# Performance work log

Measured on AMD Instinct MI355X. Metric: run time of the kernel, lower is better.

Reference implementation:

```python
import jax, jax.numpy as jnp
import numpy as np

FP16_MIN = -65504.0  # torch.finfo(torch.float16).min


def addcoords(x):
    # x: (b, c, h, w) NCHW. AddCoords(rank=1, with_r=True): appends a
    # y-coordinate channel (normalized over h, broadcast over w) and |y-0.5|.
    b, c, h, w = x.shape
    yy = (jnp.arange(h, dtype=x.dtype) / (h - 1)) * 2.0 - 1.0  # (h,)
    yy = jnp.broadcast_to(yy[None, None, :, None], (b, 1, h, w))
    rr = jnp.abs(yy - 0.5)
    return jnp.concatenate([x, yy, rr], axis=1)


def conv1x1(x, W, b):
    # W: (c_out, c_in), b: (c_out,)
    return jnp.einsum('bihw,oi->bohw', x, W) + b[None, :, None, None]


def setup_inputs() -> dict:
    key = jax.random.key(0)
    ks = jax.random.split(key, 16)
    c = 64
    B2, h, w = 4, 256, 256
    s_in = 0.02
    inp = {
        'x': jax.random.normal(ks[0], (B2, c, h, w), jnp.float32),
        'res_enc': jax.random.normal(ks[1], (B2, c, h, w), jnp.float32),
        'tr_feat': jax.random.normal(ks[2], (B2, c, h, w), jnp.float32),
        # CoordConv 1x1 weights take c+2 input channels (coord + r channels)
        'Wl1': jax.random.normal(ks[3], (c, c + 2), jnp.float32) * s_in,
        'bl1': jax.random.normal(ks[4], (c,), jnp.float32) * s_in,
        'Wr1': jax.random.normal(ks[5], (c, c + 2), jnp.float32) * s_in,
        'br1': jax.random.normal(ks[6], (c,), jnp.float32) * s_in,
        'Wl2': jax.random.normal(ks[7], (c, c), jnp.float32) * s_in,
        'bl2': jax.random.normal(ks[8], (c,), jnp.float32) * s_in,
        'Wr2': jax.random.normal(ks[9], (c, c), jnp.float32) * s_in,
        'br2': jax.random.normal(ks[10], (c,), jnp.float32) * s_in,
        'beta1': jax.random.normal(ks[11], (1, c, 1, 1), jnp.float32) * s_in,
        'gamma1': jax.random.normal(ks[12], (1, c, 1, 1), jnp.float32) * s_in,
        'beta3': jax.random.normal(ks[13], (1, c, 1, 1), jnp.float32) * s_in,
        'gamma3': jax.random.normal(ks[14], (1, c, 1, 1), jnp.float32) * s_in,
    }
    return inp


def reference(x, res_enc, tr_feat, Wl1, bl1, Wr1, br1, Wl2, bl2, Wr2, br2,
              beta1, gamma1, beta3, gamma3):
    x_l, x_r = jnp.split(x, 2, axis=0)
    re_l, re_r = jnp.split(res_enc, 2, axis=0)
    tr_l, tr_r = jnp.split(tr_feat, 2, axis=0)
    b, c, h, w = x_l.shape
    scale = jnp.asarray(c, x.dtype) ** -0.5

    Q = conv1x1(addcoords(x_l), Wl1, bl1) + beta1 * tr_l   # (b, c, h, w)
    S = conv1x1(addcoords(x_r), Wr1, br1) + beta1 * tr_r   # (b, c, h, w)

    # per-row (epipolar) attention along width: score[b,h,i,j]
    score = jnp.einsum('bchi,bchj->bhij', Q, S) * scale
    idx = jnp.arange(w)
    upper = idx[None, :] > idx[:, None]  # strict upper triangle (j > i)
    score = jnp.where(upper[None, None], FP16_MIN, score)
    # In torch, score_T is a view of score; after in-place masking, score_T
    # masked at strict-lower positions == transpose of masked score.
    M_r2l = jax.nn.softmax(score, axis=-1)                       # (b,h,w,w)
    M_l2r = jax.nn.softmax(jnp.swapaxes(score, -1, -2), axis=-1)  # (b,h,w,w)

    buf_R = conv1x1(x_r, Wr2, br2) + gamma1 * re_r  # (b, c, h, w)
    buf_l = jnp.einsum('bhij,bchj->bchi', M_r2l, buf_R)
    buf_L = conv1x1(x_l, Wl2, bl2) + gamma1 * re_l
    buf_r = jnp.einsum('bhij,bchj->bchi', M_l2r, buf_L)

    out_L = x_l + beta3 * buf_l
    out_R = x_r + gamma3 * buf_r
    return jnp.concatenate([out_L, out_R], axis=0)
```

## Files before the change

### kernel.cpp

```cpp
#include <hip/hip_runtime.h>
#include <stdint.h>

#define HW 65536
#define C_ 64

typedef __attribute__((ext_vector_type(8))) short short8;
typedef __attribute__((ext_vector_type(4))) float f32x4;

#define MFMA(a, b, c) __builtin_amdgcn_mfma_f32_16x16x32_bf16((a), (b), (c), 0, 0, 0)

union U16x8 { uint4 q; short8 v; uint32_t u[4]; };

__device__ inline uint32_t pack_bf16(float lo, float hi) {
  uint32_t ul = __float_as_uint(lo), uh = __float_as_uint(hi);
  ul = (ul + 0x7fffu + ((ul >> 16) & 1u)) >> 16;
  uh = (uh + 0x7fffu + ((uh >> 16) & 1u)) >> 16;
  return ul | (uh << 16);
}
__device__ inline uint16_t bf16r(float f) {
  uint32_t u = __float_as_uint(f);
  return (uint16_t)((u + 0x7fffu + ((u >> 16) & 1u)) >> 16);
}
__device__ inline short8 ld8(const uint16_t* p) {
  U16x8 t; t.q = *(const uint4*)p; return t.v;
}
__device__ inline int pc_idx(int pixel, int c) {
  return (pixel * 64 + c) ^ ((pixel & 7) << 3);
}
__device__ inline int cj_idx(int c, int j) {
  return (c * 256 + j) ^ ((c & 7) << 3);
}

__global__ __launch_bounds__(512, 1) void SCAM_73151882985874_kernel(
    const float* __restrict__ x, const float* __restrict__ res_enc,
    const float* __restrict__ tr_feat,
    const float* __restrict__ Wl1, const float* __restrict__ bl1,
    const float* __restrict__ Wr1, const float* __restrict__ br1,
    const float* __restrict__ Wl2, const float* __restrict__ bl2,
    const float* __restrict__ Wr2, const float* __restrict__ br2,
    const float* __restrict__ beta1, const float* __restrict__ gamma1,
    const float* __restrict__ beta3, const float* __restrict__ gamma3,
    float* __restrict__ out)
{
  __shared__ uint16_t sX[16384];
  __shared__ uint16_t sQ[16384];
  __shared__ uint16_t sS[16384];
  __shared__ uint16_t sV[16384];
  __shared__ uint16_t sP[10240];

  const int tid = threadIdx.x;
  const int wid = tid >> 6, lane = tid & 63, g = lane >> 4, li = lane & 15;
  const int bb = blockIdx.x >> 8, hh = blockIdx.x & 255;
  const float yy = (float)hh * (2.0f / 255.0f) - 1.0f;
  const float rr = fabsf(yy - 0.5f);

  const size_t rowoff = (size_t)hh * 256;
  const float* xl  = x + ((size_t)bb * C_) * HW + rowoff;
  const float* xr  = x + ((size_t)(2 + bb) * C_) * HW + rowoff;
  const float* trl = tr_feat + ((size_t)bb * C_) * HW + rowoff;
  const float* trr = tr_feat + ((size_t)(2 + bb) * C_) * HW + rowoff;
  const float* rel = res_enc + ((size_t)bb * C_) * HW + rowoff;
  const float* rer = res_enc + ((size_t)(2 + bb) * C_) * HW + rowoff;
  float* outL = out + ((size_t)bb * C_) * HW + rowoff;
  float* outR = out + ((size_t)(2 + bb) * C_) * HW + rowoff;

  uint16_t* Pw = &sP[wid * 1280];

  auto stage = [&](const float* src) {
    int p = tid & 255, h = tid >> 8;
    #pragma unroll
    for (int cb = 0; cb < 4; ++cb) {
      int c0 = h * 32 + cb * 8;
      const float* s = src + (size_t)c0 * HW + p;
      U16x8 t;
      t.u[0] = pack_bf16(s[0],              s[(size_t)HW]);
      t.u[1] = pack_bf16(s[2 * (size_t)HW], s[3 * (size_t)HW]);
      t.u[2] = pack_bf16(s[4 * (size_t)HW], s[5 * (size_t)HW]);
      t.u[3] = pack_bf16(s[6 * (size_t)HW], s[7 * (size_t)HW]);
      *(uint4*)&sX[pc_idx(p, c0)] = t.q;
    }
  };

  auto conv = [&](const float* Wm, int ldw, const float* bias, const float* mod,
                  const float* E, int coord, float qscale,
                  uint16_t* dstQ , int toV) {
    short8 af[4][2];
    #pragma unroll
    for (int ct = 0; ct < 4; ++ct)
      #pragma unroll
      for (int kk = 0; kk < 2; ++kk) {
        const float* wr = Wm + (size_t)(ct * 16 + li) * ldw + kk * 32 + g * 8;
        U16x8 t;
        t.u[0] = pack_bf16(wr[0], wr[1]);
        t.u[1] = pack_bf16(wr[2], wr[3]);
        t.u[2] = pack_bf16(wr[4], wr[5]);
        t.u[3] = pack_bf16(wr[6], wr[7]);
        af[ct][kk] = t.v;
      }
    #pragma unroll
    for (int ptl = 0; ptl < 2; ++ptl) {
      int pix = (wid * 2 + ptl) * 16 + li;
      short8 bx0 = ld8(&sX[pc_idx(pix, g * 8)]);
      short8 bx1 = ld8(&sX[pc_idx(pix, 32 + g * 8)]);
      #pragma unroll
      for (int ct = 0; ct < 4; ++ct) {
        f32x4 acc = {0.f, 0.f, 0.f, 0.f};
        acc = MFMA(af[ct][0], bx0, acc);
        acc = MFMA(af[ct][1], bx1, acc);
        uint16_t pk[4];
        #pragma unroll
        for (int r = 0; r < 4; ++r) {
          int c = ct * 16 + 4 * g + r;
          float b = bias[c];
          if (coord) b += Wm[(size_t)c * ldw + 64] * yy + Wm[(size_t)c * ldw + 65] * rr;
          float v = (acc[r] + b + mod[c] * E[(size_t)c * HW + pix]) * qscale;
          pk[r] = bf16r(v);
          if (toV) sV[cj_idx(c, pix)] = pk[r];
        }
        if (!toV) {
          uint2 w2;
          w2.x = (uint32_t)pk[0] | ((uint32_t)pk[1] << 16);
          w2.y = (uint32_t)pk[2] | ((uint32_t)pk[3] << 16);
          *(uint2*)&dstQ[pc_idx(pix, ct * 16 + 4 * g)] = w2;
        }
      }
    }
  };

  stage(xl);
  __syncthreads();
  conv(Wl1, 66, bl1, beta1, trl, 1, 0.125f, sQ, 0);
  conv(Wl2, 64, bl2, gamma1, rel, 0, 1.0f, nullptr, 1);
  __syncthreads();
  stage(xr);
  __syncthreads();
  conv(Wr1, 66, br1, beta1, trr, 1, 1.0f, sS, 0);
  __syncthreads();

  {
    const int j0 = wid * 32;
    short8 bS[2][2];
    #pragma unroll
    for (int jt = 0; jt < 2; ++jt)
      #pragma unroll
      for (int kk = 0; kk < 2; ++kk)
        bS[jt][kk] = ld8(&sS[pc_idx(j0 + jt * 16 + li, kk * 32 + g * 8)]);

    f32x4 acc[4][2];
    #pragma unroll
    for (int ct = 0; ct < 4; ++ct) { acc[ct][0] = (f32x4){0,0,0,0}; acc[ct][1] = (f32x4){0,0,0,0}; }
    float zp0 = 0.f, zp1 = 0.f;

    for (int ip = wid; ip < 8; ++ip) {
      #pragma unroll
      for (int itl = 0; itl < 2; ++itl) {
        short8 aQ0 = ld8(&sQ[pc_idx(ip * 32 + itl * 16 + li, g * 8)]);
        short8 aQ1 = ld8(&sQ[pc_idx(ip * 32 + itl * 16 + li, 32 + g * 8)]);
        #pragma unroll
        for (int jt = 0; jt < 2; ++jt) {
          f32x4 s = {0.f, 0.f, 0.f, 0.f};
          s = MFMA(aQ0, bS[jt][0], s);
          s = MFMA(aQ1, bS[jt][1], s);
          int jj = j0 + jt * 16 + li;
          float ps = 0.f; uint16_t pk[4];
          #pragma unroll
          for (int r = 0; r < 4; ++r) {
            int ii = ip * 32 + itl * 16 + 4 * g + r;
            float p = (ii >= jj) ? __expf(s[r]) : 0.f;
            ps += p; pk[r] = bf16r(p);
          }
          if (jt == 0) zp0 += ps; else zp1 += ps;
          uint2 w2;
          w2.x = (uint32_t)pk[0] | ((uint32_t)pk[1] << 16);
          w2.y = (uint32_t)pk[2] | ((uint32_t)pk[3] << 16);
          *(uint2*)&Pw[(jt * 16 + li) * 40 + itl * 16 + 4 * g] = w2;
        }
      }
      #pragma unroll
      for (int jt = 0; jt < 2; ++jt) {
        short8 bP = ld8(&Pw[(jt * 16 + li) * 40 + 8 * g]);
        #pragma unroll
        for (int ct = 0; ct < 4; ++ct) {
          short8 aV = ld8(&sV[cj_idx(ct * 16 + li, ip * 32 + 8 * g)]);
          acc[ct][jt] = MFMA(aV, bP, acc[ct][jt]);
        }
      }
    }
    zp0 += __shfl_xor(zp0, 16); zp0 += __shfl_xor(zp0, 32);
    zp1 += __shfl_xor(zp1, 16); zp1 += __shfl_xor(zp1, 32);
    #pragma unroll
    for (int jt = 0; jt < 2; ++jt) {
      float invz = 1.0f / (jt == 0 ? zp0 : zp1);
      int j = j0 + jt * 16 + li;
      #pragma unroll
      for (int ct = 0; ct < 4; ++ct)
        #pragma unroll
        for (int r = 0; r < 4; ++r) {
          int c = ct * 16 + 4 * g + r;
          outR[(size_t)c * HW + j] =
              fmaf(gamma3[c], acc[ct][jt][r] * invz, xr[(size_t)c * HW + j]);
        }
    }
  }
  __syncthreads();
  conv(Wr2, 64, br2, gamma1, rer, 0, 1.0f, nullptr, 1);
  __syncthreads();

  {
    const int i0 = wid * 32;
    short8 bQ[2][2];
    #pragma unroll
    for (int itl = 0; itl < 2; ++itl)
      #pragma unroll
      for (int kk = 0; kk < 2; ++kk)
        bQ[itl][kk] = ld8(&sQ[pc_idx(i0 + itl * 16 + li, kk * 32 + g * 8)]);

    f32x4 acc[4][2];
    #pragma unroll
    for (int ct = 0; ct < 4; ++ct) { acc[ct][0] = (f32x4){0,0,0,0}; acc[ct][1] = (f32x4){0,0,0,0}; }
    float zp0 = 0.f, zp1 = 0.f;

    for (int jp = 0; jp <= wid; ++jp) {
      #pragma unroll
      for (int jt = 0; jt < 2; ++jt) {
        short8 aS0 = ld8(&sS[pc_idx(jp * 32 + jt * 16 + li, g * 8)]);
        short8 aS1 = ld8(&sS[pc_idx(jp * 32 + jt * 16 + li, 32 + g * 8)]);
        #pragma unroll
        for (int itl = 0; itl < 2; ++itl) {
          f32x4 s = {0.f, 0.f, 0.f, 0.f};
          s = MFMA(aS0, bQ[itl][0], s);
          s = MFMA(aS1, bQ[itl][1], s);
          int ii = i0 + itl * 16 + li;
          float ps = 0.f; uint16_t pk[4];
          #pragma unroll
          for (int r = 0; r < 4; ++r) {
            int jj = jp * 32 + jt * 16 + 4 * g + r;
            float p = (jj <= ii) ? __expf(s[r]) : 0.f;
            ps += p; pk[r] = bf16r(p);
          }
          if (itl == 0) zp0 += ps; else zp1 += ps;
          uint2 w2;
          w2.x = (uint32_t)pk[0] | ((uint32_t)pk[1] << 16);
          w2.y = (uint32_t)pk[2] | ((uint32_t)pk[3] << 16);
          *(uint2*)&Pw[(itl * 16 + li) * 40 + jt * 16 + 4 * g] = w2;
        }
      }
      #pragma unroll
      for (int itl = 0; itl < 2; ++itl) {
        short8 bP = ld8(&Pw[(itl * 16 + li) * 40 + 8 * g]);
        #pragma unroll
        for (int ct = 0; ct < 4; ++ct) {
          short8 aV = ld8(&sV[cj_idx(ct * 16 + li, jp * 32 + 8 * g)]);
          acc[ct][itl] = MFMA(aV, bP, acc[ct][itl]);
        }
      }
    }
    zp0 += __shfl_xor(zp0, 16); zp0 += __shfl_xor(zp0, 32);
    zp1 += __shfl_xor(zp1, 16); zp1 += __shfl_xor(zp1, 32);
    #pragma unroll
    for (int itl = 0; itl < 2; ++itl) {
      float invz = 1.0f / (itl == 0 ? zp0 : zp1);
      int i = i0 + itl * 16 + li;
      #pragma unroll
      for (int ct = 0; ct < 4; ++ct)
        #pragma unroll
        for (int r = 0; r < 4; ++r) {
          int c = ct * 16 + 4 * g + r;
          outL[(size_t)c * HW + i] =
              fmaf(beta3[c], acc[ct][itl][r] * invz, xl[(size_t)c * HW + i]);
        }
    }
  }
}

extern "C" void kernel_launch(void* const* d_in, const int* in_sizes, int n_in,
                              void* d_out, int out_size, void* d_ws, size_t ws_size,
                              hipStream_t stream) {
  const float* x       = (const float*)d_in[0];
  const float* res_enc = (const float*)d_in[1];
  const float* tr_feat = (const float*)d_in[2];
  const float* Wl1     = (const float*)d_in[3];
  const float* bl1     = (const float*)d_in[4];
  const float* Wr1     = (const float*)d_in[5];
  const float* br1     = (const float*)d_in[6];
  const float* Wl2     = (const float*)d_in[7];
  const float* bl2     = (const float*)d_in[8];
  const float* Wr2     = (const float*)d_in[9];
  const float* br2     = (const float*)d_in[10];
  const float* beta1   = (const float*)d_in[11];
  const float* gamma1  = (const float*)d_in[12];
  const float* beta3   = (const float*)d_in[13];
  const float* gamma3  = (const float*)d_in[14];
  float* outp = (float*)d_out;

  dim3 grid(512);
  dim3 block(512);
  SCAM_73151882985874_kernel<<<grid, block, 0, stream>>>(
      x, res_enc, tr_feat, Wl1, bl1, Wr1, br1, Wl2, bl2, Wr2, br2,
      beta1, gamma1, beta3, gamma3, outp);
}
```

Measured before the change: 86.53 us.

## Use 1024-thread blocks with one 16-pixel tile per wave and merged phases

Doubles the block to 1024 threads so each wave handles a single 16-pixel tile. Both x_l and x_r are staged into shared memory at once, and all four 1x1 convolutions run in one phase, with Q and S written in place over the staged inputs. This drops several block-wide barriers and the second staging pass, and adds more waves per CU to hide latency. In exchange it uses more registers per CU, the causal triangle work is split less evenly across waves, and the launch bound now asks for 4 blocks per CU, which the shared-memory footprint may not permit.

After: 106.3 us. 22.9% more time.

```diff
diff --git a/kernel.cpp b/kernel.cpp
--- a/kernel.cpp
+++ b/kernel.cpp
@@ -31,7 +31,7 @@
   return (c * 256 + j) ^ ((c & 7) << 3);
 }
 
-__global__ __launch_bounds__(512, 1) void SCAM_73151882985874_kernel(
+__global__ __launch_bounds__(1024, 4) void SCAM_73151882985874_kernel(
     const float* __restrict__ x, const float* __restrict__ res_enc,
     const float* __restrict__ tr_feat,
     const float* __restrict__ Wl1, const float* __restrict__ bl1,
@@ -42,10 +42,10 @@
     const float* __restrict__ beta3, const float* __restrict__ gamma3,
     float* __restrict__ out)
 {
-  __shared__ uint16_t sX[16384];
-  __shared__ uint16_t sQ[16384];
-  __shared__ uint16_t sS[16384];
-  __shared__ uint16_t sV[16384];
+  __shared__ uint16_t R1[16384];
+  __shared__ uint16_t R2[16384];
+  __shared__ uint16_t R3[16384];
+  __shared__ uint16_t R4[16384];
   __shared__ uint16_t sP[10240];
 
   const int tid = threadIdx.x;
@@ -64,212 +64,180 @@
   float* outL = out + ((size_t)bb * C_) * HW + rowoff;
   float* outR = out + ((size_t)(2 + bb) * C_) * HW + rowoff;
 
-  uint16_t* Pw = &sP[wid * 1280];
-
-  auto stage = [&](const float* src) {
-    int p = tid & 255, h = tid >> 8;
+  {
+    const int side = tid >> 9;
+    const int t    = tid & 511;
+    const int p    = t & 255, h2 = t >> 8;
+    const float* src = side ? xr : xl;
+    uint16_t* dst = side ? R2 : R1;
     #pragma unroll
     for (int cb = 0; cb < 4; ++cb) {
-      int c0 = h * 32 + cb * 8;
+      int c0 = h2 * 32 + cb * 8;
       const float* s = src + (size_t)c0 * HW + p;
-      U16x8 t;
-      t.u[0] = pack_bf16(s[0],              s[(size_t)HW]);
-      t.u[1] = pack_bf16(s[2 * (size_t)HW], s[3 * (size_t)HW]);
-      t.u[2] = pack_bf16(s[4 * (size_t)HW], s[5 * (size_t)HW]);
-      t.u[3] = pack_bf16(s[6 * (size_t)HW], s[7 * (size_t)HW]);
-      *(uint4*)&sX[pc_idx(p, c0)] = t.q;
+      U16x8 t8;
+      t8.u[0] = pack_bf16(s[0],              s[(size_t)HW]);
+      t8.u[1] = pack_bf16(s[2 * (size_t)HW], s[3 * (size_t)HW]);
+      t8.u[2] = pack_bf16(s[4 * (size_t)HW], s[5 * (size_t)HW]);
+      t8.u[3] = pack_bf16(s[6 * (size_t)HW], s[7 * (size_t)HW]);
+      *(uint4*)&dst[pc_idx(p, c0)] = t8.q;
+    }
+  }
+  __syncthreads();
+
+  const int pix = wid * 16 + li;
+
+  short8 bxL0 = ld8(&R1[pc_idx(pix, g * 8)]);
+  short8 bxL1 = ld8(&R1[pc_idx(pix, 32 + g * 8)]);
+  short8 bxR0 = ld8(&R2[pc_idx(pix, g * 8)]);
+  short8 bxR1 = ld8(&R2[pc_idx(pix, 32 + g * 8)]);
+
+  auto conv_one = [&](const float* __restrict__ Wm, int ldw,
+                      const float* __restrict__ bias, const float* __restrict__ mod,
+                      const float* __restrict__ E, int coord, float qscale,
+                      short8 bx0, short8 bx1,
+                      uint16_t* dstPC, uint16_t* dstV) {
+    #pragma unroll
+    for (int ct = 0; ct < 4; ++ct) {
+      float ev[4], be[4];
+      #pragma unroll
+      for (int r = 0; r < 4; ++r) {
+        int c = ct * 16 + 4 * g + r;
+        ev[r] = E[(size_t)c * HW + pix];
+        float b = bias[c] + mod[c] * 0.0f;
+        if (coord) b += Wm[(size_t)c * ldw + 64] * yy + Wm[(size_t)c * ldw + 65] * rr;
+        be[r] = b;
+      }
+      float md[4];
+      #pragma unroll
+      for (int r = 0; r < 4; ++r) md[r] = mod[ct * 16 + 4 * g + r];
+      short8 af0, af1;
+      {
+        const float* wr = Wm + (size_t)(ct * 16 + li) * ldw + g * 8;
+        U16x8 t8;
+        t8.u[0] = pack_bf16(wr[0], wr[1]); t8.u[1] = pack_bf16(wr[2], wr[3]);
+        t8.u[2] = pack_bf16(wr[4], wr[5]); t8.u[3] = pack_bf16(wr[6], wr[7]);
+        af0 = t8.v;
+        const float* wr2 = wr + 32;
+        t8.u[0] = pack_bf16(wr2[0], wr2[1]); t8.u[1] = pack_bf16(wr2[2], wr2[3]);
+        t8.u[2] = pack_bf16(wr2[4], wr2[5]); t8.u[3] = pack_bf16(wr2[6], wr2[7]);
+        af1 = t8.v;
+      }
+      f32x4 acc = {0.f, 0.f, 0.f, 0.f};
+      acc = MFMA(af0, bx0, acc);
+      acc = MFMA(af1, bx1, acc);
+      uint16_t pk[4];
+      #pragma unroll
+      for (int r = 0; r < 4; ++r)
+        pk[r] = bf16r((acc[r] + be[r] + md[r] * ev[r]) * qscale);
+      if (dstV) {
+        #pragma unroll
+        for (int r = 0; r < 4; ++r) dstV[cj_idx(ct * 16 + 4 * g + r, pix)] = pk[r];
+      } else {
+        uint2 w2;
+        w2.x = (uint32_t)pk[0] | ((uint32_t)pk[1] << 16);
+        w2.y = (uint32_t)pk[2] | ((uint32_t)pk[3] << 16);
+        *(uint2*)&dstPC[pc_idx(pix, ct * 16 + 4 * g)] = w2;
+      }
     }
   };
 
-  auto conv = [&](const float* Wm, int ldw, const float* bias, const float* mod,
-                  const float* E, int coord, float qscale,
-                  uint16_t* dstQ , int toV) {
-    short8 af[4][2];
-    #pragma unroll
-    for (int ct = 0; ct < 4; ++ct)
-      #pragma unroll
-      for (int kk = 0; kk < 2; ++kk) {
-        const float* wr = Wm + (size_t)(ct * 16 + li) * ldw + kk * 32 + g * 8;
-        U16x8 t;
-        t.u[0] = pack_bf16(wr[0], wr[1]);
-        t.u[1] = pack_bf16(wr[2], wr[3]);
-        t.u[2] = pack_bf16(wr[4], wr[5]);
-        t.u[3] = pack_bf16(wr[6], wr[7]);
-        af[ct][kk] = t.v;
-      }
-    #pragma unroll
-    for (int ptl = 0; ptl < 2; ++ptl) {
-      int pix = (wid * 2 + ptl) * 16 + li;
-      short8 bx0 = ld8(&sX[pc_idx(pix, g * 8)]);
-      short8 bx1 = ld8(&sX[pc_idx(pix, 32 + g * 8)]);
-      #pragma unroll
-      for (int ct = 0; ct < 4; ++ct) {
-        f32x4 acc = {0.f, 0.f, 0.f, 0.f};
-        acc = MFMA(af[ct][0], bx0, acc);
-        acc = MFMA(af[ct][1], bx1, acc);
+  conv_one(Wl1, 66, bl1, beta1, trl, 1, 0.125f, bxL0, bxL1, R1, nullptr);
+  conv_one(Wr1, 66, br1, beta1, trr, 1, 1.0f,   bxR0, bxR1, R2, nullptr);
+  conv_one(Wl2, 64, bl2, gamma1, rel, 0, 1.0f,  bxL0, bxL1, nullptr, R3);
+  conv_one(Wr2, 64, br2, gamma1, rer, 0, 1.0f,  bxR0, bxR1, nullptr, R4);
+  __syncthreads();
+
+  uint16_t* Pw = &sP[wid * 640];
+  const int h = wid >> 1;
+
+  {
+    short8 bS0 = ld8(&R2[pc_idx(pix, g * 8)]);
+    short8 bS1 = ld8(&R2[pc_idx(pix, 32 + g * 8)]);
+    f32x4 acc[4] = {{0,0,0,0},{0,0,0,0},{0,0,0,0},{0,0,0,0}};
+    float z = 0.f;
+    for (int ip = h; ip < 8; ++ip) {
+      #pragma unroll
+      for (int itl = 0; itl < 2; ++itl) {
+        int arow = ip * 32 + itl * 16 + li;
+        short8 aQ0 = ld8(&R1[pc_idx(arow, g * 8)]);
+        short8 aQ1 = ld8(&R1[pc_idx(arow, 32 + g * 8)]);
+        f32x4 s = {0.f, 0.f, 0.f, 0.f};
+        s = MFMA(aQ0, bS0, s);
+        s = MFMA(aQ1, bS1, s);
         uint16_t pk[4];
         #pragma unroll
         for (int r = 0; r < 4; ++r) {
-          int c = ct * 16 + 4 * g + r;
-          float b = bias[c];
-          if (coord) b += Wm[(size_t)c * ldw + 64] * yy + Wm[(size_t)c * ldw + 65] * rr;
-          float v = (acc[r] + b + mod[c] * E[(size_t)c * HW + pix]) * qscale;
-          pk[r] = bf16r(v);
-          if (toV) sV[cj_idx(c, pix)] = pk[r];
+          int aidx = ip * 32 + itl * 16 + 4 * g + r;
+          float p = (aidx >= pix) ? __expf(s[r]) : 0.f;
+          z += p; pk[r] = bf16r(p);
         }
-        if (!toV) {
-          uint2 w2;
-          w2.x = (uint32_t)pk[0] | ((uint32_t)pk[1] << 16);
-          w2.y = (uint32_t)pk[2] | ((uint32_t)pk[3] << 16);
-          *(uint2*)&dstQ[pc_idx(pix, ct * 16 + 4 * g)] = w2;
-        }
-      }
-    }
-  };
-
-  stage(xl);
-  __syncthreads();
-  conv(Wl1, 66, bl1, beta1, trl, 1, 0.125f, sQ, 0);
-  conv(Wl2, 64, bl2, gamma1, rel, 0, 1.0f, nullptr, 1);
-  __syncthreads();
-  stage(xr);
-  __syncthreads();
-  conv(Wr1, 66, br1, beta1, trr, 1, 1.0f, sS, 0);
-  __syncthreads();
+        uint2 w2;
+        w2.x = (uint32_t)pk[0] | ((uint32_t)pk[1] << 16);
+        w2.y = (uint32_t)pk[2] | ((uint32_t)pk[3] << 16);
+        *(uint2*)&Pw[li * 40 + itl * 16 + 4 * g] = w2;
+      }
+      short8 bP = ld8(&Pw[li * 40 + 8 * g]);
+      #pragma unroll
+      for (int ct = 0; ct < 4; ++ct) {
+        short8 aV = ld8(&R3[cj_idx(ct * 16 + li, ip * 32 + 8 * g)]);
+        acc[ct] = MFMA(aV, bP, acc[ct]);
+      }
+    }
+    z += __shfl_xor(z, 16); z += __shfl_xor(z, 32);
+    float invz = 1.0f / z;
+    #pragma unroll
+    for (int ct = 0; ct < 4; ++ct)
+      #pragma unroll
+      for (int r = 0; r < 4; ++r) {
+        int c = ct * 16 + 4 * g + r;
+        outR[(size_t)c * HW + pix] =
+            fmaf(gamma3[c], acc[ct][r] * invz, xr[(size_t)c * HW + pix]);
+      }
+  }
 
   {
-    const int j0 = wid * 32;
-    short8 bS[2][2];
-    #pragma unroll
-    for (int jt = 0; jt < 2; ++jt)
-      #pragma unroll
-      for (int kk = 0; kk < 2; ++kk)
-        bS[jt][kk] = ld8(&sS[pc_idx(j0 + jt * 16 + li, kk * 32 + g * 8)]);
-
-    f32x4 acc[4][2];
-    #pragma unroll
-    for (int ct = 0; ct < 4; ++ct) { acc[ct][0] = (f32x4){0,0,0,0}; acc[ct][1] = (f32x4){0,0,0,0}; }
-    float zp0 = 0.f, zp1 = 0.f;
-
-    for (int ip = wid; ip < 8; ++ip) {
+    short8 bQ0 = ld8(&R1[pc_idx(pix, g * 8)]);
+    short8 bQ1 = ld8(&R1[pc_idx(pix, 32 + g * 8)]);
+    f32x4 acc[4] = {{0,0,0,0},{0,0,0,0},{0,0,0,0},{0,0,0,0}};
+    float z = 0.f;
+    for (int jp = 0; jp <= h; ++jp) {
       #pragma unroll
       for (int itl = 0; itl < 2; ++itl) {
-        short8 aQ0 = ld8(&sQ[pc_idx(ip * 32 + itl * 16 + li, g * 8)]);
-        short8 aQ1 = ld8(&sQ[pc_idx(ip * 32 + itl * 16 + li, 32 + g * 8)]);
-        #pragma unroll
-        for (int jt = 0; jt < 2; ++jt) {
-          f32x4 s = {0.f, 0.f, 0.f, 0.f};
-          s = MFMA(aQ0, bS[jt][0], s);
-          s = MFMA(aQ1, bS[jt][1], s);
-          int jj = j0 + jt * 16 + li;
-          float ps = 0.f; uint16_t pk[4];
-          #pragma unroll
-          for (int r = 0; r < 4; ++r) {
-            int ii = ip * 32 + itl * 16 + 4 * g + r;
-            float p = (ii >= jj) ? __expf(s[r]) : 0.f;
-            ps += p; pk[r] = bf16r(p);
-          }
-          if (jt == 0) zp0 += ps; else zp1 += ps;
-          uint2 w2;
-          w2.x = (uint32_t)pk[0] | ((uint32_t)pk[1] << 16);
-          w2.y = (uint32_t)pk[2] | ((uint32_t)pk[3] << 16);
-          *(uint2*)&Pw[(jt * 16 + li) * 40 + itl * 16 + 4 * g] = w2;
-        }
-      }
-      #pragma unroll
-      for (int jt = 0; jt < 2; ++jt) {
-        short8 bP = ld8(&Pw[(jt * 16 + li) * 40 + 8 * g]);
-        #pragma unroll
-        for (int ct = 0; ct < 4; ++ct) {
-          short8 aV = ld8(&sV[cj_idx(ct * 16 + li, ip * 32 + 8 * g)]);
-          acc[ct][jt] = MFMA(aV, bP, acc[ct][jt]);
-        }
-      }
-    }
-    zp0 += __shfl_xor(zp0, 16); zp0 += __shfl_xor(zp0, 32);
-    zp1 += __shfl_xor(zp1, 16); zp1 += __shfl_xor(zp1, 32);
-    #pragma unroll
-    for (int jt = 0; jt < 2; ++jt) {
-      float invz = 1.0f / (jt == 0 ? zp0 : zp1);
-      int j = j0 + jt * 16 + li;
-      #pragma unroll
-      for (int ct = 0; ct < 4; ++ct)
+        int arow = jp * 32 + itl * 16 + li;
+        short8 aS0 = ld8(&R2[pc_idx(arow, g * 8)]);
+        short8 aS1 = ld8(&R2[pc_idx(arow, 32 + g * 8)]);
+        f32x4 s = {0.f, 0.f, 0.f, 0.f};
+        s = MFMA(aS0, bQ0, s);
+        s = MFMA(aS1, bQ1, s);
+        uint16_t pk[4];
         #pragma unroll
         for (int r = 0; r < 4; ++r) {
-          int c = ct * 16 + 4 * g + r;
-          outR[(size_t)c * HW + j] =
-              fmaf(gamma3[c], acc[ct][jt][r] * invz, xr[(size_t)c * HW + j]);
+          int jidx = jp * 32 + itl * 16 + 4 * g + r;
+          float p = (jidx <= pix) ? __expf(s[r]) : 0.f;
+          z += p; pk[r] = bf16r(p);
         }
-    }
-  }
-  __syncthreads();
-  conv(Wr2, 64, br2, gamma1, rer, 0, 1.0f, nullptr, 1);
-  __syncthreads();
-
-  {
-    const int i0 = wid * 32;
-    short8 bQ[2][2];
-    #pragma unroll
-    for (int itl = 0; itl < 2; ++itl)
-      #pragma unroll
-      for (int kk = 0; kk < 2; ++kk)
-        bQ[itl][kk] = ld8(&sQ[pc_idx(i0 + itl * 16 + li, kk * 32 + g * 8)]);
-
-    f32x4 acc[4][2];
-    #pragma unroll
-    for (int ct = 0; ct < 4; ++ct) { acc[ct][0] = (f32x4){0,0,0,0}; acc[ct][1] = (f32x4){0,0,0,0}; }
-    float zp0 = 0.f, zp1 = 0.f;
-
-    for (int jp = 0; jp <= wid; ++jp) {
-      #pragma unroll
-      for (int jt = 0; jt < 2; ++jt) {
-        short8 aS0 = ld8(&sS[pc_idx(jp * 32 + jt * 16 + li, g * 8)]);
-        short8 aS1 = ld8(&sS[pc_idx(jp * 32 + jt * 16 + li, 32 + g * 8)]);
-        #pragma unroll
-        for (int itl = 0; itl < 2; ++itl) {
-          f32x4 s = {0.f, 0.f, 0.f, 0.f};
-          s = MFMA(aS0, bQ[itl][0], s);
-          s = MFMA(aS1, bQ[itl][1], s);
-          int ii = i0 + itl * 16 + li;
-          float ps = 0.f; uint16_t pk[4];
-          #pragma unroll
-          for (int r = 0; r < 4; ++r) {
-            int jj = jp * 32 + jt * 16 + 4 * g + r;
-            float p = (jj <= ii) ? __expf(s[r]) : 0.f;
-            ps += p; pk[r] = bf16r(p);
-          }
-          if (itl == 0) zp0 += ps; else zp1 += ps;
-          uint2 w2;
-          w2.x = (uint32_t)pk[0] | ((uint32_t)pk[1] << 16);
-          w2.y = (uint32_t)pk[2] | ((uint32_t)pk[3] << 16);
-          *(uint2*)&Pw[(itl * 16 + li) * 40 + jt * 16 + 4 * g] = w2;
-        }
-      }
-      #pragma unroll
-      for (int itl = 0; itl < 2; ++itl) {
-        short8 bP = ld8(&Pw[(itl * 16 + li) * 40 + 8 * g]);
-        #pragma unroll
-        for (int ct = 0; ct < 4; ++ct) {
-          short8 aV = ld8(&sV[cj_idx(ct * 16 + li, jp * 32 + 8 * g)]);
-          acc[ct][itl] = MFMA(aV, bP, acc[ct][itl]);
-        }
-      }
-    }
-    zp0 += __shfl_xor(zp0, 16); zp0 += __shfl_xor(zp0, 32);
-    zp1 += __shfl_xor(zp1, 16); zp1 += __shfl_xor(zp1, 32);
-    #pragma unroll
-    for (int itl = 0; itl < 2; ++itl) {
-      float invz = 1.0f / (itl == 0 ? zp0 : zp1);
-      int i = i0 + itl * 16 + li;
-      #pragma unroll
-      for (int ct = 0; ct < 4; ++ct)
-        #pragma unroll
-        for (int r = 0; r < 4; ++r) {
-          int c = ct * 16 + 4 * g + r;
-          outL[(size_t)c * HW + i] =
-              fmaf(beta3[c], acc[ct][itl][r] * invz, xl[(size_t)c * HW + i]);
-        }
-    }
+        uint2 w2;
+        w2.x = (uint32_t)pk[0] | ((uint32_t)pk[1] << 16);
+        w2.y = (uint32_t)pk[2] | ((uint32_t)pk[3] << 16);
+        *(uint2*)&Pw[li * 40 + itl * 16 + 4 * g] = w2;
+      }
+      short8 bP = ld8(&Pw[li * 40 + 8 * g]);
+      #pragma unroll
+      for (int ct = 0; ct < 4; ++ct) {
+        short8 aV = ld8(&R4[cj_idx(ct * 16 + li, jp * 32 + 8 * g)]);
+        acc[ct] = MFMA(aV, bP, acc[ct]);
+      }
+    }
+    z += __shfl_xor(z, 16); z += __shfl_xor(z, 32);
+    float invz = 1.0f / z;
+    #pragma unroll
+    for (int ct = 0; ct < 4; ++ct)
+      #pragma unroll
+      for (int r = 0; r < 4; ++r) {
+        int c = ct * 16 + 4 * g + r;
+        outL[(size_t)c * HW + pix] =
+            fmaf(beta3[c], acc[ct][r] * invz, xl[(size_t)c * HW + pix]);
+      }
   }
 }
 
@@ -294,7 +262,7 @@
   float* outp = (float*)d_out;
 
   dim3 grid(512);
-  dim3 block(512);
+  dim3 block(1024);
   SCAM_73151882985874_kernel<<<grid, block, 0, stream>>>(
       x, res_enc, tr_feat, Wl1, bl1, Wr1, br1, Wl2, bl2, Wr2, br2,
       beta1, gamma1, beta3, gamma3, outp);
```

## Prepack bf16 weights, stage both sides at once, compute all convs upfront

Applied to the files above, without the earlier changes.

Adds a small pre-kernel that converts the four conv weight matrices to bf16 in workspace, so the main kernel loads them directly instead of converting per block. Both x_l and x_r are staged into shared memory concurrently, and all four 1x1 convs are computed before attention, which removes several block-wide barriers and the mid-kernel conv. It also hoists the bias and modulation loads, batches the A/V fragment loads in the attention loops, and raises launch bounds to 2 blocks per CU. The cost is an extra launch and higher register pressure under the tighter launch bound. LDS use (about 148 KB per block) may still allow only one block per CU.

Result: slower. 92.60 us (+7.0%).

```diff
diff --git a/kernel.cpp b/kernel.cpp
--- a/kernel.cpp
+++ b/kernel.cpp
@@ -31,7 +31,18 @@
   return (c * 256 + j) ^ ((c & 7) << 3);
 }
 
-__global__ __launch_bounds__(512, 1) void SCAM_73151882985874_kernel(
+__global__ void SCAM_pack_w(const float* __restrict__ Wl1, const float* __restrict__ Wr1,
+                            const float* __restrict__ Wl2, const float* __restrict__ Wr2,
+                            uint16_t* __restrict__ ws) {
+  int idx = blockIdx.x * 256 + threadIdx.x;
+  int r = idx >> 6, k = idx & 63;
+  ws[idx]         = bf16r(Wl1[r * 66 + k]);
+  ws[4096 + idx]  = bf16r(Wr1[r * 66 + k]);
+  ws[8192 + idx]  = bf16r(Wl2[r * 64 + k]);
+  ws[12288 + idx] = bf16r(Wr2[r * 64 + k]);
+}
+
+__global__ __launch_bounds__(512, 2) void SCAM_73151882985874_kernel(
     const float* __restrict__ x, const float* __restrict__ res_enc,
     const float* __restrict__ tr_feat,
     const float* __restrict__ Wl1, const float* __restrict__ bl1,
@@ -40,12 +51,13 @@
     const float* __restrict__ Wr2, const float* __restrict__ br2,
     const float* __restrict__ beta1, const float* __restrict__ gamma1,
     const float* __restrict__ beta3, const float* __restrict__ gamma3,
+    const uint16_t* __restrict__ wsW,
     float* __restrict__ out)
 {
-  __shared__ uint16_t sX[16384];
-  __shared__ uint16_t sQ[16384];
-  __shared__ uint16_t sS[16384];
-  __shared__ uint16_t sV[16384];
+  __shared__ uint16_t R1[16384];
+  __shared__ uint16_t R2[16384];
+  __shared__ uint16_t R3[16384];
+  __shared__ uint16_t R4[16384];
   __shared__ uint16_t sP[10240];
 
   const int tid = threadIdx.x;
@@ -64,109 +76,129 @@
   float* outL = out + ((size_t)bb * C_) * HW + rowoff;
   float* outR = out + ((size_t)(2 + bb) * C_) * HW + rowoff;
 
-  uint16_t* Pw = &sP[wid * 1280];
-
-  auto stage = [&](const float* src) {
-    int p = tid & 255, h = tid >> 8;
-    #pragma unroll
-    for (int cb = 0; cb < 4; ++cb) {
-      int c0 = h * 32 + cb * 8;
+  {
+    const int side = tid >> 8;
+    const int p    = tid & 255;
+    const float* src = side ? xr : xl;
+    uint16_t* dst = side ? R2 : R1;
+    #pragma unroll
+    for (int cb = 0; cb < 8; ++cb) {
+      int c0 = cb * 8;
       const float* s = src + (size_t)c0 * HW + p;
-      U16x8 t;
-      t.u[0] = pack_bf16(s[0],              s[(size_t)HW]);
-      t.u[1] = pack_bf16(s[2 * (size_t)HW], s[3 * (size_t)HW]);
-      t.u[2] = pack_bf16(s[4 * (size_t)HW], s[5 * (size_t)HW]);
-      t.u[3] = pack_bf16(s[6 * (size_t)HW], s[7 * (size_t)HW]);
-      *(uint4*)&sX[pc_idx(p, c0)] = t.q;
-    }
-  };
-
-  auto conv = [&](const float* Wm, int ldw, const float* bias, const float* mod,
-                  const float* E, int coord, float qscale,
-                  uint16_t* dstQ , int toV) {
+      U16x8 t8;
+      t8.u[0] = pack_bf16(s[0],              s[(size_t)HW]);
+      t8.u[1] = pack_bf16(s[2 * (size_t)HW], s[3 * (size_t)HW]);
+      t8.u[2] = pack_bf16(s[4 * (size_t)HW], s[5 * (size_t)HW]);
+      t8.u[3] = pack_bf16(s[6 * (size_t)HW], s[7 * (size_t)HW]);
+      *(uint4*)&dst[pc_idx(p, c0)] = t8.q;
+    }
+  }
+  __syncthreads();
+
+  short8 bxL[2][2], bxR[2][2];
+  #pragma unroll
+  for (int ptl = 0; ptl < 2; ++ptl) {
+    int pix = wid * 32 + ptl * 16 + li;
+    bxL[ptl][0] = ld8(&R1[pc_idx(pix, g * 8)]);
+    bxL[ptl][1] = ld8(&R1[pc_idx(pix, 32 + g * 8)]);
+    bxR[ptl][0] = ld8(&R2[pc_idx(pix, g * 8)]);
+    bxR[ptl][1] = ld8(&R2[pc_idx(pix, 32 + g * 8)]);
+  }
+
+  auto conv_one = [&](const uint16_t* __restrict__ wcore,
+                      const float* __restrict__ Wc,
+                      const float* __restrict__ bias, const float* __restrict__ mod,
+                      const float* __restrict__ E, float qscale,
+                      const short8 bx[2][2], uint16_t* dstPC, uint16_t* dstV) {
     short8 af[4][2];
     #pragma unroll
+    for (int ct = 0; ct < 4; ++ct) {
+      const uint16_t* wr = wcore + (size_t)(ct * 16 + li) * 64 + g * 8;
+      af[ct][0] = ld8(wr);
+      af[ct][1] = ld8(wr + 32);
+    }
+    float be[4][4], md[4][4];
+    #pragma unroll
     for (int ct = 0; ct < 4; ++ct)
       #pragma unroll
-      for (int kk = 0; kk < 2; ++kk) {
-        const float* wr = Wm + (size_t)(ct * 16 + li) * ldw + kk * 32 + g * 8;
-        U16x8 t;
-        t.u[0] = pack_bf16(wr[0], wr[1]);
-        t.u[1] = pack_bf16(wr[2], wr[3]);
-        t.u[2] = pack_bf16(wr[4], wr[5]);
-        t.u[3] = pack_bf16(wr[6], wr[7]);
-        af[ct][kk] = t.v;
+      for (int r = 0; r < 4; ++r) {
+        int c = ct * 16 + 4 * g + r;
+        float b = bias[c];
+        if (Wc) b += Wc[(size_t)c * 66 + 64] * yy + Wc[(size_t)c * 66 + 65] * rr;
+        be[ct][r] = b;
+        md[ct][r] = mod[c];
       }
     #pragma unroll
     for (int ptl = 0; ptl < 2; ++ptl) {
-      int pix = (wid * 2 + ptl) * 16 + li;
-      short8 bx0 = ld8(&sX[pc_idx(pix, g * 8)]);
-      short8 bx1 = ld8(&sX[pc_idx(pix, 32 + g * 8)]);
+      int pix = wid * 32 + ptl * 16 + li;
       #pragma unroll
       for (int ct = 0; ct < 4; ++ct) {
+        float ev[4];
+        #pragma unroll
+        for (int r = 0; r < 4; ++r)
+          ev[r] = E[(size_t)(ct * 16 + 4 * g + r) * HW + pix];
         f32x4 acc = {0.f, 0.f, 0.f, 0.f};
-        acc = MFMA(af[ct][0], bx0, acc);
-        acc = MFMA(af[ct][1], bx1, acc);
+        acc = MFMA(af[ct][0], bx[ptl][0], acc);
+        acc = MFMA(af[ct][1], bx[ptl][1], acc);
         uint16_t pk[4];
         #pragma unroll
-        for (int r = 0; r < 4; ++r) {
-          int c = ct * 16 + 4 * g + r;
-          float b = bias[c];
-          if (coord) b += Wm[(size_t)c * ldw + 64] * yy + Wm[(size_t)c * ldw + 65] * rr;
-          float v = (acc[r] + b + mod[c] * E[(size_t)c * HW + pix]) * qscale;
-          pk[r] = bf16r(v);
-          if (toV) sV[cj_idx(c, pix)] = pk[r];
-        }
-        if (!toV) {
+        for (int r = 0; r < 4; ++r)
+          pk[r] = bf16r((acc[r] + be[ct][r] + md[ct][r] * ev[r]) * qscale);
+        if (dstV) {
+          #pragma unroll
+          for (int r = 0; r < 4; ++r) dstV[cj_idx(ct * 16 + 4 * g + r, pix)] = pk[r];
+        } else {
           uint2 w2;
           w2.x = (uint32_t)pk[0] | ((uint32_t)pk[1] << 16);
           w2.y = (uint32_t)pk[2] | ((uint32_t)pk[3] << 16);
-          *(uint2*)&dstQ[pc_idx(pix, ct * 16 + 4 * g)] = w2;
+          *(uint2*)&dstPC[pc_idx(pix, ct * 16 + 4 * g)] = w2;
         }
       }
     }
   };
 
-  stage(xl);
+  conv_one(wsW,         Wl1, bl1, beta1,  trl, 0.125f, bxL, R1, nullptr);
+  conv_one(wsW + 4096,  Wr1, br1, beta1,  trr, 1.0f,   bxR, R2, nullptr);
+  conv_one(wsW + 8192,  nullptr, bl2, gamma1, rel, 1.0f, bxL, nullptr, R3);
+  conv_one(wsW + 12288, nullptr, br2, gamma1, rer, 1.0f, bxR, nullptr, R4);
   __syncthreads();
-  conv(Wl1, 66, bl1, beta1, trl, 1, 0.125f, sQ, 0);
-  conv(Wl2, 64, bl2, gamma1, rel, 0, 1.0f, nullptr, 1);
-  __syncthreads();
-  stage(xr);
-  __syncthreads();
-  conv(Wr1, 66, br1, beta1, trr, 1, 1.0f, sS, 0);
-  __syncthreads();
+
+  uint16_t* Pw = &sP[wid * 1280];
+  const int j0 = wid * 32;
 
   {
-    const int j0 = wid * 32;
     short8 bS[2][2];
     #pragma unroll
-    for (int jt = 0; jt < 2; ++jt)
-      #pragma unroll
-      for (int kk = 0; kk < 2; ++kk)
-        bS[jt][kk] = ld8(&sS[pc_idx(j0 + jt * 16 + li, kk * 32 + g * 8)]);
-
+    for (int jt = 0; jt < 2; ++jt) {
+      bS[jt][0] = ld8(&R2[pc_idx(j0 + jt * 16 + li, g * 8)]);
+      bS[jt][1] = ld8(&R2[pc_idx(j0 + jt * 16 + li, 32 + g * 8)]);
+    }
     f32x4 acc[4][2];
     #pragma unroll
     for (int ct = 0; ct < 4; ++ct) { acc[ct][0] = (f32x4){0,0,0,0}; acc[ct][1] = (f32x4){0,0,0,0}; }
     float zp0 = 0.f, zp1 = 0.f;
 
     for (int ip = wid; ip < 8; ++ip) {
+      short8 aQ[2][2];
       #pragma unroll
       for (int itl = 0; itl < 2; ++itl) {
-        short8 aQ0 = ld8(&sQ[pc_idx(ip * 32 + itl * 16 + li, g * 8)]);
-        short8 aQ1 = ld8(&sQ[pc_idx(ip * 32 + itl * 16 + li, 32 + g * 8)]);
+        int arow = ip * 32 + itl * 16 + li;
+        aQ[itl][0] = ld8(&R1[pc_idx(arow, g * 8)]);
+        aQ[itl][1] = ld8(&R1[pc_idx(arow, 32 + g * 8)]);
+      }
+      #pragma unroll
+      for (int itl = 0; itl < 2; ++itl)
         #pragma unroll
         for (int jt = 0; jt < 2; ++jt) {
           f32x4 s = {0.f, 0.f, 0.f, 0.f};
-          s = MFMA(aQ0, bS[jt][0], s);
-          s = MFMA(aQ1, bS[jt][1], s);
+          s = MFMA(aQ[itl][0], bS[jt][0], s);
+          s = MFMA(aQ[itl][1], bS[jt][1], s);
           int jj = j0 + jt * 16 + li;
           float ps = 0.f; uint16_t pk[4];
           #pragma unroll
           for (int r = 0; r < 4; ++r) {
-            int ii = ip * 32 + itl * 16 + 4 * g + r;
-            float p = (ii >= jj) ? __expf(s[r]) : 0.f;
+            int aidx = ip * 32 + itl * 16 + 4 * g + r;
+            float p = (aidx >= jj) ? __expf(s[r]) : 0.f;
             ps += p; pk[r] = bf16r(p);
           }
           if (jt == 0) zp0 += ps; else zp1 += ps;
@@ -175,15 +207,16 @@
           w2.y = (uint32_t)pk[2] | ((uint32_t)pk[3] << 16);
           *(uint2*)&Pw[(jt * 16 + li) * 40 + itl * 16 + 4 * g] = w2;
         }
-      }
+      short8 aV[4];
+      #pragma unroll
+      for (int ct = 0; ct < 4; ++ct)
+        aV[ct] = ld8(&R3[cj_idx(ct * 16 + li, ip * 32 + 8 * g)]);
       #pragma unroll
       for (int jt = 0; jt < 2; ++jt) {
         short8 bP = ld8(&Pw[(jt * 16 + li) * 40 + 8 * g]);
         #pragma unroll
-        for (int ct = 0; ct < 4; ++ct) {
-          short8 aV = ld8(&sV[cj_idx(ct * 16 + li, ip * 32 + 8 * g)]);
-          acc[ct][jt] = MFMA(aV, bP, acc[ct][jt]);
-        }
+        for (int ct = 0; ct < 4; ++ct)
+          acc[ct][jt] = MFMA(aV[ct], bP, acc[ct][jt]);
       }
     }
     zp0 += __shfl_xor(zp0, 16); zp0 += __shfl_xor(zp0, 32);
@@ -202,57 +235,58 @@
         }
     }
   }
-  __syncthreads();
-  conv(Wr2, 64, br2, gamma1, rer, 0, 1.0f, nullptr, 1);
-  __syncthreads();
 
   {
-    const int i0 = wid * 32;
     short8 bQ[2][2];
     #pragma unroll
-    for (int itl = 0; itl < 2; ++itl)
-      #pragma unroll
-      for (int kk = 0; kk < 2; ++kk)
-        bQ[itl][kk] = ld8(&sQ[pc_idx(i0 + itl * 16 + li, kk * 32 + g * 8)]);
-
+    for (int itl = 0; itl < 2; ++itl) {
+      bQ[itl][0] = ld8(&R1[pc_idx(j0 + itl * 16 + li, g * 8)]);
+      bQ[itl][1] = ld8(&R1[pc_idx(j0 + itl * 16 + li, 32 + g * 8)]);
+    }
     f32x4 acc[4][2];
     #pragma unroll
     for (int ct = 0; ct < 4; ++ct) { acc[ct][0] = (f32x4){0,0,0,0}; acc[ct][1] = (f32x4){0,0,0,0}; }
     float zp0 = 0.f, zp1 = 0.f;
 
     for (int jp = 0; jp <= wid; ++jp) {
-      #pragma unroll
-      for (int jt = 0; jt < 2; ++jt) {
-        short8 aS0 = ld8(&sS[pc_idx(jp * 32 + jt * 16 + li, g * 8)]);
-        short8 aS1 = ld8(&sS[pc_idx(jp * 32 + jt * 16 + li, 32 + g * 8)]);
+      short8 aS[2][2];
+      #pragma unroll
+      for (int jtl = 0; jtl < 2; ++jtl) {
+        int arow = jp * 32 + jtl * 16 + li;
+        aS[jtl][0] = ld8(&R2[pc_idx(arow, g * 8)]);
+        aS[jtl][1] = ld8(&R2[pc_idx(arow, 32 + g * 8)]);
+      }
+      #pragma unroll
+      for (int jtl = 0; jtl < 2; ++jtl)
         #pragma unroll
         for (int itl = 0; itl < 2; ++itl) {
           f32x4 s = {0.f, 0.f, 0.f, 0.f};
-          s = MFMA(aS0, bQ[itl][0], s);
-          s = MFMA(aS1, bQ[itl][1], s);
-          int ii = i0 + itl * 16 + li;
+          s = MFMA(aS[jtl][0], bQ[itl][0], s);
+          s = MFMA(aS[jtl][1], bQ[itl][1], s);
+          int ii = j0 + itl * 16 + li;
           float ps = 0.f; uint16_t pk[4];
           #pragma unroll
           for (int r = 0; r < 4; ++r) {
-            int jj = jp * 32 + jt * 16 + 4 * g + r;
-            float p = (jj <= ii) ? __expf(s[r]) : 0.f;
+            int jidx = jp * 32 + jtl * 16 + 4 * g + r;
+            float p = (jidx <= ii) ? __expf(s[r]) : 0.f;
             ps += p; pk[r] = bf16r(p);
           }
           if (itl == 0) zp0 += ps; else zp1 += ps;
           uint2 w2;
           w2.x = (uint32_t)pk[0] | ((uint32_t)pk[1] << 16);
           w2.y = (uint32_t)pk[2] | ((uint32_t)pk[3] << 16);
-          *(uint2*)&Pw[(itl * 16 + li) * 40 + jt * 16 + 4 * g] = w2;
-        }
-      }
+          *(uint2*)&Pw[(itl * 16 + li) * 40 + jtl * 16 + 4 * g] = w2;
+        }
+      short8 aV[4];
+      #pragma unroll
+      for (int ct = 0; ct < 4; ++ct)
+        aV[ct] = ld8(&R4[cj_idx(ct * 16 + li, jp * 32 + 8 * g)]);
       #pragma unroll
       for (int itl = 0; itl < 2; ++itl) {
         short8 bP = ld8(&Pw[(itl * 16 + li) * 40 + 8 * g]);
         #pragma unroll
-        for (int ct = 0; ct < 4; ++ct) {
-          short8 aV = ld8(&sV[cj_idx(ct * 16 + li, jp * 32 + 8 * g)]);
-          acc[ct][itl] = MFMA(aV, bP, acc[ct][itl]);
-        }
+        for (int ct = 0; ct < 4; ++ct)
+          acc[ct][itl] = MFMA(aV[ct], bP, acc[ct][itl]);
       }
     }
     zp0 += __shfl_xor(zp0, 16); zp0 += __shfl_xor(zp0, 32);
@@ -260,7 +294,7 @@
     #pragma unroll
     for (int itl = 0; itl < 2; ++itl) {
       float invz = 1.0f / (itl == 0 ? zp0 : zp1);
-      int i = i0 + itl * 16 + li;
+      int i = j0 + itl * 16 + li;
       #pragma unroll
       for (int ct = 0; ct < 4; ++ct)
         #pragma unroll
@@ -292,10 +326,13 @@
   const float* beta3   = (const float*)d_in[13];
   const float* gamma3  = (const float*)d_in[14];
   float* outp = (float*)d_out;
+  uint16_t* wsW = (uint16_t*)d_ws;
+
+  SCAM_pack_w<<<dim3(16), dim3(256), 0, stream>>>(Wl1, Wr1, Wl2, Wr2, wsW);
 
   dim3 grid(512);
   dim3 block(512);
   SCAM_73151882985874_kernel<<<grid, block, 0, stream>>>(
       x, res_enc, tr_feat, Wl1, bl1, Wr1, br1, Wl2, bl2, Wr2, br2,
-      beta1, gamma1, beta3, gamma3, outp);
-}
+      beta1, gamma1, beta3, gamma3, wsW, outp);
+}
```
